# Performance work log

Measured on AMD Instinct MI355X. Metric: run time of the kernel, lower is better.

Reference implementation:

```python
import jax, jax.numpy as jnp
import numpy as np

N_USERS = 100000
N_ITEMS = 50000
N_EDGES = 1000000
IN_FEAT = 64
HID_FEAT = 64
R = 5


def setup_inputs() -> dict:
    key = jax.random.key(0)
    k1, k2, k3, k4, k5, k6 = jax.random.split(key, 6)
    return {
        "user_x": jax.random.normal(k1, (N_USERS, IN_FEAT), dtype=jnp.float32),
        "item_x": jax.random.normal(k2, (N_ITEMS, IN_FEAT), dtype=jnp.float32),
        "weight": jax.random.normal(k3, (R, IN_FEAT, HID_FEAT), dtype=jnp.float32),
        "u_s": jax.random.randint(k4, (N_EDGES,), 0, N_USERS, dtype=jnp.int32),
        "v_s": jax.random.randint(k5, (N_EDGES,), 0, N_ITEMS, dtype=jnp.int32),
        "rate": jax.random.randint(k6, (N_EDGES,), 0, R, dtype=jnp.int32),
    }


def _aggregate(src_x, weight, src_idx, dst_idx, rate, n_dst):
    # Transform at node level (cheap), then gather per edge: [N_src, R, H] -> [E, H]
    xw = jnp.einsum('ni,rio->nro', src_x, weight)
    msg = xw[src_idx, rate]                     # [E, H]
    # c_ij = number of edges at dst node with the same rating
    n_r = weight.shape[0]
    key = dst_idx * n_r + rate
    cnt = jax.ops.segment_sum(jnp.ones_like(rate, dtype=msg.dtype), key,
                              num_segments=n_dst * n_r)
    c = cnt[key]                                # [E], >= 1 for existing edges
    return jax.ops.segment_sum(msg / c[:, None], dst_idx, num_segments=n_dst)


def reference(user_x, item_x, weight, u_s, v_s, rate):
    # w_sharing=False, activation=None, dropout=0.0 (eval)
    h_u = _aggregate(item_x, weight, v_s, u_s, rate, user_x.shape[0])  # items -> users
    h_v = _aggregate(user_x, weight, u_s, v_s, rate, item_x.shape[0])  # users -> items
    return h_u, h_v
```

## Files before the change

kernel.cpp:

```cpp
#include <hip/hip_runtime.h>


constexpr int FEAT  = 64;
constexpr int RC    = 5;
constexpr int STRIP = 16;
constexpr int CHUNK = 50000;

__global__ __launch_bounds__(256) void build_links(
    const int* __restrict__ u_s, const int* __restrict__ v_s,
    int* __restrict__ head_u, int* __restrict__ head_v,
    int* __restrict__ next_u, int* __restrict__ next_v, int n_edges)
{
  const int e = blockIdx.x * blockDim.x + threadIdx.x;
  if (e >= n_edges) return;
  next_u[e] = atomicExch(&head_u[u_s[e]], e);
  next_v[e] = atomicExch(&head_v[v_s[e]], e);
}

__global__ __launch_bounds__(256) void aggregate_dir(
    const float* __restrict__ src_x,
    const int* __restrict__ src_idx,
    const int* __restrict__ rate,
    const int* __restrict__ head,
    const int* __restrict__ next,
    float* __restrict__ accum,
    int node_base, int node_count)
{
  const int lane = threadIdx.x & 63;
  const int w    = (blockIdx.x * blockDim.x + threadIdx.x) >> 6;
  if (w >= node_count) return;
  const int d = node_base + w;

  float a0 = 0.f, a1 = 0.f, a2 = 0.f, a3 = 0.f, a4 = 0.f;
  int   c0 = 0,   c1 = 0,   c2 = 0,   c3 = 0,   c4 = 0;

  for (int e = head[d]; e >= 0; e = next[e]) {
    const int s = src_idx[e];
    const int r = rate[e];
    const float xv = src_x[(size_t)s * FEAT + lane];
    a0 += (r == 0) ? xv : 0.f;  c0 += (r == 0);
    a1 += (r == 1) ? xv : 0.f;  c1 += (r == 1);
    a2 += (r == 2) ? xv : 0.f;  c2 += (r == 2);
    a3 += (r == 3) ? xv : 0.f;  c3 += (r == 3);
    a4 += (r == 4) ? xv : 0.f;  c4 += (r == 4);
  }

  float* row = accum + (size_t)w * RC * FEAT + lane;
  row[0 * FEAT] = a0 / (float)(c0 > 0 ? c0 : 1);
  row[1 * FEAT] = a1 / (float)(c1 > 0 ? c1 : 1);
  row[2 * FEAT] = a2 / (float)(c2 > 0 ? c2 : 1);
  row[3 * FEAT] = a3 / (float)(c3 > 0 ? c3 : 1);
  row[4 * FEAT] = a4 / (float)(c4 > 0 ? c4 : 1);
}

__global__ __launch_bounds__(256) void transform_v3(
    const float* __restrict__ accum,
    const float* __restrict__ W,
    float* __restrict__ out,
    int node_count)
{
  const int lane = threadIdx.x & 63;
  const int wid  = (blockIdx.x * blockDim.x + threadIdx.x) >> 6;
  const int nw   = (gridDim.x * blockDim.x) >> 6;

  for (int base = wid * STRIP; base < node_count; base += nw * STRIP) {
    const int base_u = __builtin_amdgcn_readfirstlane(base);
    float o_acc[STRIP];
#pragma unroll
    for (int n = 0; n < STRIP; ++n) o_acc[n] = 0.f;

    for (int r = 0; r < RC; ++r) {
      float wcol[FEAT];
#pragma unroll
      for (int k = 0; k < FEAT; ++k)
        wcol[k] = W[((size_t)r * FEAT + k) * FEAT + lane];

#pragma unroll
      for (int n = 0; n < STRIP; ++n) {
        const int node = base_u + n;
        if (node >= node_count) break;
        const float4* ap4 = reinterpret_cast<const float4*>(
            accum + ((size_t)node * RC + r) * FEAT);
        float t = 0.f;
#pragma unroll
        for (int k4 = 0; k4 < FEAT / 4; ++k4) {
          const float4 a = ap4[k4];
          t = fmaf(a.x, wcol[k4 * 4 + 0], t);
          t = fmaf(a.y, wcol[k4 * 4 + 1], t);
          t = fmaf(a.z, wcol[k4 * 4 + 2], t);
          t = fmaf(a.w, wcol[k4 * 4 + 3], t);
        }
        o_acc[n] += t;
      }
    }
#pragma unroll
    for (int n = 0; n < STRIP; ++n) {
      if (base + n < node_count)
        out[(size_t)(base + n) * FEAT + lane] = o_acc[n];
    }
  }
}

extern "C" void kernel_launch(void* const* d_in, const int* in_sizes, int n_in,
                              void* d_out, int out_size, void* d_ws, size_t ws_size,
                              hipStream_t stream) {
  const float* user_x = (const float*)d_in[0];
  const float* item_x = (const float*)d_in[1];
  const float* weight = (const float*)d_in[2];
  const int*   u_s    = (const int*)d_in[3];
  const int*   v_s    = (const int*)d_in[4];
  const int*   rate   = (const int*)d_in[5];

  const int n_users = in_sizes[0] / FEAT;
  const int n_items = in_sizes[1] / FEAT;
  const int n_edges = in_sizes[3];

  float* out = (float*)d_out;
  float* h_u = out;
  float* h_v = out + (size_t)n_users * FEAT;

  float* accum  = (float*)d_ws;
  int*   head_u = (int*)(accum + (size_t)CHUNK * RC * FEAT);
  int*   head_v = head_u + n_users;
  int*   next_u = head_v + n_items;
  int*   next_v = next_u + n_edges;

  hipMemsetAsync(head_u, 0xFF, (size_t)(n_users + n_items) * sizeof(int), stream);

  build_links<<<(n_edges + 255) / 256, 256, 0, stream>>>(
      u_s, v_s, head_u, head_v, next_u, next_v, n_edges);

  for (int base = 0; base < n_users; base += CHUNK) {
    const int cnt = (n_users - base < CHUNK) ? (n_users - base) : CHUNK;
    aggregate_dir<<<(cnt + 3) / 4, 256, 0, stream>>>(
        item_x, v_s, rate, head_u, next_u, accum, base, cnt);
    transform_v3<<<(cnt + 63) / 64, 256, 0, stream>>>(
        accum, weight, h_u + (size_t)base * FEAT, cnt);
  }

  for (int base = 0; base < n_items; base += CHUNK) {
    const int cnt = (n_items - base < CHUNK) ? (n_items - base) : CHUNK;
    aggregate_dir<<<(cnt + 3) / 4, 256, 0, stream>>>(
        user_x, u_s, rate, head_v, next_v, accum, base, cnt);
    transform_v3<<<(cnt + 63) / 64, 256, 0, stream>>>(
        accum, weight, h_v + (size_t)base * FEAT, cnt);
  }

  (void)ws_size; (void)n_in; (void)out_size;
}
```

Measured before the change: 627.9 us.

## Replace per-node linked edge lists with CSR built by histogram and scan

Edge adjacency was a linked list built with atomicExch, where each aggregation step waited on a dependent load of next[e], then src_idx[e] and rate[e]. It is now a CSR layout built with a degree histogram, a three-kernel prefix scan and an atomic fill. Each entry packs source index and rating into one int, so aggregation reads a contiguous, independent stream of edge entries instead of chasing pointers. The cost is more preprocessing launches (histogram, scans, fill) and a second pass of edge atomics. The packing also assumes node indices fit in 29 bits.

```diff
diff --git a/kernel.cpp b/kernel.cpp
--- a/kernel.cpp
+++ b/kernel.cpp
@@ -6,37 +6,104 @@
 constexpr int STRIP = 16;
 constexpr int CHUNK = 50000;
 
-__global__ __launch_bounds__(256) void build_links(
+__global__ __launch_bounds__(256) void hist(
     const int* __restrict__ u_s, const int* __restrict__ v_s,
-    int* __restrict__ head_u, int* __restrict__ head_v,
-    int* __restrict__ next_u, int* __restrict__ next_v, int n_edges)
+    int* __restrict__ cnt_u, int* __restrict__ cnt_v, int n_edges)
 {
   const int e = blockIdx.x * blockDim.x + threadIdx.x;
   if (e >= n_edges) return;
-  next_u[e] = atomicExch(&head_u[u_s[e]], e);
-  next_v[e] = atomicExch(&head_v[v_s[e]], e);
-}
-
-__global__ __launch_bounds__(256) void aggregate_dir(
+  atomicAdd(&cnt_u[u_s[e]], 1);
+  atomicAdd(&cnt_v[v_s[e]], 1);
+}
+
+__global__ __launch_bounds__(256) void scan1(
+    const int* __restrict__ in, int* __restrict__ out_local,
+    int* __restrict__ bsum, int n)
+{
+  __shared__ int s[256];
+  const int tid = threadIdx.x;
+  const int i = blockIdx.x * 256 + tid;
+  const int v = (i < n) ? in[i] : 0;
+  s[tid] = v; __syncthreads();
+#pragma unroll
+  for (int off = 1; off < 256; off <<= 1) {
+    const int t = (tid >= off) ? s[tid - off] : 0;
+    __syncthreads();
+    s[tid] += t;
+    __syncthreads();
+  }
+  if (i < n) out_local[i] = s[tid] - v;
+  if (tid == 255) bsum[blockIdx.x] = s[255];
+}
+
+__global__ __launch_bounds__(256) void scan2(int* __restrict__ bsum, int nb)
+{
+  __shared__ int s[256];
+  const int tid = threadIdx.x;
+  int carry = 0;
+  for (int start = 0; start < nb; start += 256) {
+    const int i = start + tid;
+    const int v = (i < nb) ? bsum[i] : 0;
+    s[tid] = v; __syncthreads();
+#pragma unroll
+    for (int off = 1; off < 256; off <<= 1) {
+      const int t = (tid >= off) ? s[tid - off] : 0;
+      __syncthreads();
+      s[tid] += t;
+      __syncthreads();
+    }
+    const int total = s[255];
+    if (i < nb) bsum[i] = carry + s[tid] - v;
+    carry += total;
+    __syncthreads();
+  }
+}
+
+__global__ __launch_bounds__(256) void scan3(
+    int* __restrict__ base, const int* __restrict__ bsum, int n)
+{
+  const int i = blockIdx.x * 256 + threadIdx.x;
+  if (i < n) base[i] += bsum[blockIdx.x];
+}
+
+__global__ __launch_bounds__(256) void fill_csr(
+    const int* __restrict__ u_s, const int* __restrict__ v_s,
+    const int* __restrict__ rate,
+    const int* __restrict__ base_u, const int* __restrict__ base_v,
+    int* __restrict__ cur_u, int* __restrict__ cur_v,
+    int* __restrict__ csr_u, int* __restrict__ csr_v, int n_edges)
+{
+  const int e = blockIdx.x * blockDim.x + threadIdx.x;
+  if (e >= n_edges) return;
+  const int u = u_s[e], v = v_s[e], r = rate[e];
+  const int pu = base_u[u] + atomicAdd(&cur_u[u], 1);
+  csr_u[pu] = (v << 3) | r;
+  const int pv = base_v[v] + atomicAdd(&cur_v[v], 1);
+  csr_v[pv] = (u << 3) | r;
+}
+
+__global__ __launch_bounds__(256) void aggregate_csr(
     const float* __restrict__ src_x,
-    const int* __restrict__ src_idx,
-    const int* __restrict__ rate,
-    const int* __restrict__ head,
-    const int* __restrict__ next,
+    const int* __restrict__ csr,
+    const int* __restrict__ base,
+    const int* __restrict__ cnt,
     float* __restrict__ accum,
     int node_base, int node_count)
 {
   const int lane = threadIdx.x & 63;
   const int w    = (blockIdx.x * blockDim.x + threadIdx.x) >> 6;
   if (w >= node_count) return;
-  const int d = node_base + w;
+  const int d   = node_base + w;
+  const int off = base[d];
+  const int deg = cnt[d];
 
   float a0 = 0.f, a1 = 0.f, a2 = 0.f, a3 = 0.f, a4 = 0.f;
   int   c0 = 0,   c1 = 0,   c2 = 0,   c3 = 0,   c4 = 0;
 
-  for (int e = head[d]; e >= 0; e = next[e]) {
-    const int s = src_idx[e];
-    const int r = rate[e];
+  for (int i = 0; i < deg; ++i) {
+    const unsigned p = (unsigned)csr[off + i];
+    const int s = (int)(p >> 3);
+    const int r = (int)(p & 7u);
     const float xv = src_x[(size_t)s * FEAT + lane];
     a0 += (r == 0) ? xv : 0.f;  c0 += (r == 0);
     a1 += (r == 1) ? xv : 0.f;  c1 += (r == 1);
@@ -120,30 +187,50 @@
   float* h_v = out + (size_t)n_users * FEAT;
 
   float* accum  = (float*)d_ws;
-  int*   head_u = (int*)(accum + (size_t)CHUNK * RC * FEAT);
-  int*   head_v = head_u + n_users;
-  int*   next_u = head_v + n_items;
-  int*   next_v = next_u + n_edges;
-
-  hipMemsetAsync(head_u, 0xFF, (size_t)(n_users + n_items) * sizeof(int), stream);
-
-  build_links<<<(n_edges + 255) / 256, 256, 0, stream>>>(
-      u_s, v_s, head_u, head_v, next_u, next_v, n_edges);
-
-  for (int base = 0; base < n_users; base += CHUNK) {
-    const int cnt = (n_users - base < CHUNK) ? (n_users - base) : CHUNK;
-    aggregate_dir<<<(cnt + 3) / 4, 256, 0, stream>>>(
-        item_x, v_s, rate, head_u, next_u, accum, base, cnt);
+  int*   cnt_u  = (int*)(accum + (size_t)CHUNK * RC * FEAT);
+  int*   cnt_v  = cnt_u + n_users;
+  int*   cur_u  = cnt_v + n_items;
+  int*   cur_v  = cur_u + n_users;
+  int*   base_u = cur_v + n_items;
+  int*   base_v = base_u + n_users;
+  int*   bsum_u = base_v + n_items;
+  int*   bsum_v = bsum_u + 512;
+  int*   csr_u  = bsum_v + 512;
+  int*   csr_v  = csr_u + n_edges;
+
+  const int nb_u = (n_users + 255) / 256;
+  const int nb_v = (n_items + 255) / 256;
+  const int gE   = (n_edges + 255) / 256;
+
+  hipMemsetAsync(cnt_u, 0,
+                 (size_t)2 * (n_users + n_items) * sizeof(int), stream);
+
+  hist<<<gE, 256, 0, stream>>>(u_s, v_s, cnt_u, cnt_v, n_edges);
+
+  scan1<<<nb_u, 256, 0, stream>>>(cnt_u, base_u, bsum_u, n_users);
+  scan1<<<nb_v, 256, 0, stream>>>(cnt_v, base_v, bsum_v, n_items);
+  scan2<<<1, 256, 0, stream>>>(bsum_u, nb_u);
+  scan2<<<1, 256, 0, stream>>>(bsum_v, nb_v);
+  scan3<<<nb_u, 256, 0, stream>>>(base_u, bsum_u, n_users);
+  scan3<<<nb_v, 256, 0, stream>>>(base_v, bsum_v, n_items);
+
+  fill_csr<<<gE, 256, 0, stream>>>(u_s, v_s, rate, base_u, base_v,
+                                   cur_u, cur_v, csr_u, csr_v, n_edges);
+
+  for (int cb = 0; cb < n_users; cb += CHUNK) {
+    const int cnt = (n_users - cb < CHUNK) ? (n_users - cb) : CHUNK;
+    aggregate_csr<<<(cnt + 3) / 4, 256, 0, stream>>>(
+        item_x, csr_u, base_u, cnt_u, accum, cb, cnt);
     transform_v3<<<(cnt + 63) / 64, 256, 0, stream>>>(
-        accum, weight, h_u + (size_t)base * FEAT, cnt);
-  }
-
-  for (int base = 0; base < n_items; base += CHUNK) {
-    const int cnt = (n_items - base < CHUNK) ? (n_items - base) : CHUNK;
-    aggregate_dir<<<(cnt + 3) / 4, 256, 0, stream>>>(
-        user_x, u_s, rate, head_v, next_v, accum, base, cnt);
+        accum, weight, h_u + (size_t)cb * FEAT, cnt);
+  }
+
+  for (int cb = 0; cb < n_items; cb += CHUNK) {
+    const int cnt = (n_items - cb < CHUNK) ? (n_items - cb) : CHUNK;
+    aggregate_csr<<<(cnt + 3) / 4, 256, 0, stream>>>(
+        user_x, csr_v, base_v, cnt_v, accum, cb, cnt);
     transform_v3<<<(cnt + 63) / 64, 256, 0, stream>>>(
-        accum, weight, h_v + (size_t)base * FEAT, cnt);
+        accum, weight, h_v + (size_t)cb * FEAT, cnt);
   }
 
   (void)ws_size; (void)n_in; (void)out_size;
```

After: 716.9 us. +14.2%, slower.
